# Kernel tuning notes

Hardware: AMD Instinct MI355X
Metric: run time of the kernel (lower is better)

The kernel has to match this reference:

```python
import math
import jax
import jax.numpy as jnp
import numpy as np
from jax import lax

B, L, D_MODEL, N_HEADS, C = 4, 2048, 512, 8, 1
D_HEAD = D_MODEL // N_HEADS


def setup_inputs() -> dict:
    key = jax.random.key(0)
    ks = jax.random.split(key, 7)
    s = 0.02  # stand-in for glorot init scale
    return {
        "queries": jax.random.normal(ks[0], (B, L, D_MODEL), jnp.float32),
        "keys": jax.random.normal(ks[1], (B, L, D_MODEL), jnp.float32),
        "values": jax.random.normal(ks[2], (B, L, D_MODEL), jnp.float32),
        "wq": jax.random.normal(ks[3], (D_MODEL, D_MODEL), jnp.float32) * s,
        "wk": jax.random.normal(ks[4], (D_MODEL, D_MODEL), jnp.float32) * s,
        "wv": jax.random.normal(ks[5], (D_MODEL, D_MODEL), jnp.float32) * s,
        "wo": jax.random.normal(ks[6], (D_MODEL, D_MODEL), jnp.float32) * s,
    }


def reference(queries, keys, values, wq, wk, wv, wo):
    b, len_q, _ = queries.shape
    len_k = keys.shape[1]
    # QKV projections, split into heads: [B, H, L, Dh]
    Q = (queries @ wq).reshape(b, len_q, N_HEADS, D_HEAD).transpose(0, 2, 1, 3)
    K = (keys @ wk).reshape(b, len_k, N_HEADS, D_HEAD).transpose(0, 2, 1, 3)
    V = (values @ wv).reshape(b, len_k, N_HEADS, D_HEAD).transpose(0, 2, 1, 3)
    # full O(L^2) correlation as in the original, then mean over heads & query idx
    corr = jnp.einsum("bhid,bhjd->bhij", Q, K)  # [B, H, Lq, Lk]
    mean_corr = corr.mean(axis=(1, 2))  # [B, Lk]
    # top-k delay selection (k = max(1, int(c * log(Lq))), static at trace time)
    k = max(1, int(C * math.log(max(2, len_q))))
    topk_vals, topk_idx = lax.top_k(mean_corr, k)  # [B, k]
    weights = jax.nn.softmax(topk_vals, axis=-1)  # [B, k]
    # vectorized circular roll: rolled[b,i,h,t,d] = V[b,h,(t+delay_bi) % L, d]
    idx = (jnp.arange(len_k)[None, None, :] + topk_idx[:, :, None]) % len_k  # [B,k,L]
    gathered = jnp.take_along_axis(
        V[:, None],  # [B, 1, H, L, Dh]
        idx[:, :, None, :, None],  # [B, k, 1, L, 1]
        axis=3,
    )  # [B, k, H, L, Dh]
    agg = jnp.einsum("bk,bkhld->bhld", weights.astype(V.dtype), gathered)
    out = agg.transpose(0, 2, 1, 3).reshape(b, len_q, D_MODEL) @ wo
    return out
```

## Files before the change

### kernel.cpp

```cpp
#include <hip/hip_runtime.h>
#include <hip/hip_bf16.h>

#define DMODEL 512
#define LEN 2048
#define NBATCH 4
#define TOPK 7
#define LDK 40

typedef __attribute__((ext_vector_type(8))) short short8;
typedef __attribute__((ext_vector_type(4))) float floatx4;

__device__ __forceinline__ float b2f(ushort h) {
  union { uint u; float f; } c; c.u = ((uint)h) << 16; return c.f;
}
__device__ __forceinline__ ushort f2b(float f) {
  union { float f; uint u; } c; c.f = f;
  uint u = c.u;
  uint r = (u + 0x7fffu + ((u >> 16) & 1u)) >> 16;
  return (ushort)r;
}

__device__ __forceinline__ float ld1(const void* p, size_t i, int bf) {
  return bf ? b2f(((const ushort*)p)[i]) : ((const float*)p)[i];
}
__device__ __forceinline__ void ld4v(const void* p, size_t i, int bf, float* o) {
  if (bf) {
    uint2 v = *(const uint2*)((const ushort*)p + i);
    const ushort* s = (const ushort*)&v;
#pragma unroll
    for (int j = 0; j < 4; ++j) o[j] = b2f(s[j]);
  } else {
    float4 a = *(const float4*)((const float*)p + i);
    o[0] = a.x; o[1] = a.y; o[2] = a.z; o[3] = a.w;
  }
}
__device__ __forceinline__ void ld8v(const void* p, size_t i, int bf, float* o) {
  if (bf) {
    uint4 v = *(const uint4*)((const ushort*)p + i);
    const ushort* s = (const ushort*)&v;
#pragma unroll
    for (int j = 0; j < 8; ++j) o[j] = b2f(s[j]);
  } else {
    float4 a = *(const float4*)((const float*)p + i);
    float4 b = *(const float4*)((const float*)p + i + 4);
    o[0] = a.x; o[1] = a.y; o[2] = a.z; o[3] = a.w;
    o[4] = b.x; o[5] = b.y; o[6] = b.z; o[7] = b.w;
  }
}

__device__ __forceinline__ int detect_bf16(const void* probe) {
  __shared__ int s_flag;
  int t = threadIdx.x;
  if (t < 64) {
    const uint4* p = (const uint4*)probe;
    uint4 a = p[t * 2];
    uint4 b = p[t * 2 + 1];
    uint w[8] = {a.x, a.y, a.z, a.w, b.x, b.y, b.z, b.w};
    int c = 0;
#pragma unroll
    for (int j = 0; j < 8; ++j) {
      uint e = (w[j] >> 7) & 0xFFu;
      c += (e < 90u || e > 140u) ? 1 : 0;
    }
#pragma unroll
    for (int off = 32; off > 0; off >>= 1) c += __shfl_down(c, off);
    if (t == 0) s_flag = (c < 50) ? 1 : 0;
  }
  __syncthreads();
  return s_flag;
}

__global__ __launch_bounds__(256) void prep_k(
    const void* __restrict__ queries, const void* __restrict__ values,
    const void* __restrict__ wv, const void* __restrict__ wo,
    const void* __restrict__ probe,
    float* __restrict__ P, ushort* __restrict__ VB, ushort* __restrict__ W2T) {
  __shared__ ushort As[64 * LDK];
  __shared__ ushort Bs[64 * LDK];
  __shared__ ushort Ts[64 * 72];
  int bf = detect_bf16(probe);
  int blk = blockIdx.x;
  int t = threadIdx.x;
  if (blk < 256) {
    int b = blk >> 6, c = blk & 63;
    size_t base = (((size_t)b * LEN + (size_t)c * 32) << 9) + t;
    float a0 = 0.f, a1 = 0.f;
#pragma unroll 8
    for (int l = 0; l < 32; ++l) {
      a0 += ld1(queries, base + ((size_t)l << 9), bf);
      a1 += ld1(queries, base + ((size_t)l << 9) + 256, bf);
    }
    P[(size_t)blk * DMODEL + t] = a0;
    P[(size_t)blk * DMODEL + t + 256] = a1;
  } else if (blk < 2304) {
    int r = (blk - 256) * 4 + (t >> 6);
    int lane = t & 63;
    float v[8];
    ld8v(values, ((size_t)r << 9) + lane * 8, bf, v);
    union { ushort o[8]; uint4 u; } pk;
#pragma unroll
    for (int j = 0; j < 8; ++j) pk.o[j] = f2b(v[j]);
    *(uint4*)(VB + ((size_t)r << 9) + lane * 8) = pk.u;
  } else {
    int wb = blk - 2304;
    int n0 = (wb & 7) * 64, m0 = (wb >> 3) * 64;
    int w = t >> 6, lane = t & 63;
    int quad = lane >> 4, l16 = lane & 15;
    floatx4 acc[4] = {{0,0,0,0},{0,0,0,0},{0,0,0,0},{0,0,0,0}};
    int am = t >> 2, ak = (t & 3) * 8;
    int kp = t >> 4, nb = (t & 15) * 4;
    for (int k0 = 0; k0 < DMODEL; k0 += 32) {
      float a8[8];
      ld8v(wv, (size_t)(m0 + am) * DMODEL + k0 + ak, bf, a8);
      union { ushort s[8]; uint4 v; } ap;
#pragma unroll
      for (int j = 0; j < 8; ++j) ap.s[j] = f2b(a8[j]);
      *(uint4*)(&As[am * LDK + ak]) = ap.v;
      float b0[4], b1[4];
      ld4v(wo, (size_t)(k0 + 2 * kp) * DMODEL + n0 + nb, bf, b0);
      ld4v(wo, (size_t)(k0 + 2 * kp + 1) * DMODEL + n0 + nb, bf, b1);
#pragma unroll
      for (int i = 0; i < 4; ++i) {
        ushort2 pr; pr.x = f2b(b0[i]); pr.y = f2b(b1[i]);
        *(ushort2*)(&Bs[(nb + i) * LDK + 2 * kp]) = pr;
      }
      __syncthreads();
      short8 af = *(const short8*)(&As[(w * 16 + l16) * LDK + quad * 8]);
#pragma unroll
      for (int c = 0; c < 4; ++c) {
        short8 bfr = *(const short8*)(&Bs[(c * 16 + l16) * LDK + quad * 8]);
        acc[c] = __builtin_amdgcn_mfma_f32_16x16x32_bf16(af, bfr, acc[c], 0, 0, 0);
      }
      __syncthreads();
    }
#pragma unroll
    for (int c = 0; c < 4; ++c) {
      int cl = c * 16 + l16;
#pragma unroll
      for (int r = 0; r < 4; ++r)
        Ts[cl * 72 + (w * 16 + quad * 4 + r)] = f2b(acc[c][r]);
    }
    __syncthreads();
    int nl = t >> 2, ch = t & 3;
    uint4 v0 = *(const uint4*)(&Ts[nl * 72 + ch * 16]);
    uint4 v1 = *(const uint4*)(&Ts[nl * 72 + ch * 16 + 8]);
    ushort* dst = W2T + (size_t)(n0 + nl) * DMODEL + m0 + ch * 16;
    *(uint4*)dst = v0;
    *(uint4*)(dst + 8) = v1;
  }
}

__global__ __launch_bounds__(256) void qbar_k(
    const float* __restrict__ P, const void* __restrict__ wq,
    float* __restrict__ qb) {
  __shared__ float qs[DMODEL];
  __shared__ float red[4][64];
  int bf = detect_bf16(wq);
  int b = blockIdx.x >> 3, g = blockIdx.x & 7;
  int t = threadIdx.x;
  for (int d = t; d < DMODEL; d += 256) {
    float a = 0.f;
#pragma unroll
    for (int c = 0; c < 64; ++c) a += P[(size_t)(b * 64 + c) * DMODEL + d];
    qs[d] = a;
  }
  __syncthreads();
  int part = t >> 6, jl = t & 63;
  int j = g * 64 + jl;
  float acc = 0.f;
  int d0 = part * 128;
#pragma unroll 8
  for (int d = d0; d < d0 + 128; ++d)
    acc += qs[d] * ld1(wq, (size_t)d * DMODEL + j, bf);
  red[part][jl] = acc;
  __syncthreads();
  if (part == 0)
    qb[(size_t)b * DMODEL + j] = red[0][jl] + red[1][jl] + red[2][jl] + red[3][jl];
}

__global__ __launch_bounds__(256) void u_k(
    const float* __restrict__ qb, const void* __restrict__ wk,
    float* __restrict__ u, const void* __restrict__ probe) {
  int bf = detect_bf16(probe);
  int gw = (blockIdx.x * 256 + threadIdx.x) >> 6;
  int lane = threadIdx.x & 63;
  int b = gw >> 9, t = gw & 511;
  float kv[8];
  ld8v(wk, (size_t)t * DMODEL + lane * 8, bf, kv);
  const float* qbb = qb + (size_t)b * DMODEL + lane * 8;
  float acc = 0.f;
#pragma unroll
  for (int i = 0; i < 8; ++i) acc += kv[i] * qbb[i];
#pragma unroll
  for (int off = 32; off > 0; off >>= 1) acc += __shfl_down(acc, off);
  if (lane == 0) u[(size_t)b * DMODEL + t] = acc;
}

__global__ __launch_bounds__(256) void mean_corr_k(
    const void* __restrict__ keys, const float* __restrict__ u,
    float* __restrict__ mc, const void* __restrict__ probe) {
  int bf = detect_bf16(probe);
  int wid = (blockIdx.x * 256 + threadIdx.x) >> 6;
  int lane = threadIdx.x & 63;
  int b = wid >> 11, j = wid & (LEN - 1);
  float kv[8];
  ld8v(keys, (((size_t)b * LEN + j) << 9) + lane * 8, bf, kv);
  const float* ub = u + (size_t)b * DMODEL + lane * 8;
  float acc = 0.f;
#pragma unroll
  for (int i = 0; i < 8; ++i) acc += kv[i] * ub[i];
#pragma unroll
  for (int off = 32; off > 0; off >>= 1) acc += __shfl_down(acc, off);
  if (lane == 0) mc[(size_t)b * LEN + j] = acc * (1.f / 16384.f);
}

__global__ void topk_softmax(const float* __restrict__ mc,
                             float* __restrict__ wts, int* __restrict__ dls) {
  __shared__ float vals[LEN];
  __shared__ float rv[4];
  __shared__ int ri[4];
  __shared__ float bv_s[TOPK];
  __shared__ int bi_s[TOPK];
  int b = blockIdx.x, t = threadIdx.x;
  for (int i = t; i < LEN; i += 256) vals[i] = mc[(size_t)b * LEN + i];
  __syncthreads();
  for (int it = 0; it < TOPK; ++it) {
    float bv = -3.0e38f; int bi = 0;
#pragma unroll
    for (int c = 0; c < LEN / 256; ++c) {
      int i = t + c * 256;
      float v = vals[i];
      if (v > bv) { bv = v; bi = i; }
    }
#pragma unroll
    for (int off = 32; off > 0; off >>= 1) {
      float ov = __shfl_down(bv, off);
      int   oi = __shfl_down(bi, off);
      if (ov > bv || (ov == bv && oi < bi)) { bv = ov; bi = oi; }
    }
    if ((t & 63) == 0) { rv[t >> 6] = bv; ri[t >> 6] = bi; }
    __syncthreads();
    if (t == 0) {
      float fv = rv[0]; int fi = ri[0];
      for (int w = 1; w < 4; ++w)
        if (rv[w] > fv || (rv[w] == fv && ri[w] < fi)) { fv = rv[w]; fi = ri[w]; }
      bv_s[it] = fv; bi_s[it] = fi;
      vals[fi] = -3.0e38f;
    }
    __syncthreads();
  }
  if (t == 0) {
    float m = bv_s[0];
    float e[TOPK], s = 0.f;
#pragma unroll
    for (int i = 0; i < TOPK; ++i) { e[i] = __expf(bv_s[i] - m); s += e[i]; }
    float inv = 1.f / s;
#pragma unroll
    for (int i = 0; i < TOPK; ++i) {
      wts[b * 8 + i] = e[i] * inv;
      dls[b * 8 + i] = bi_s[i];
    }
  }
}

__global__ __launch_bounds__(256) void mix_k(
    const ushort* __restrict__ VB, const float* __restrict__ wts,
    const int* __restrict__ dls, ushort* __restrict__ Amix) {
  int t = threadIdx.x;
  int row = blockIdx.x * 4 + (t >> 6);
  int lane = t & 63;
  int b = row >> 11, l = row & (LEN - 1);
  float w[TOPK]; int dl[TOPK];
#pragma unroll
  for (int i = 0; i < TOPK; ++i) { w[i] = wts[b * 8 + i]; dl[i] = dls[b * 8 + i]; }
  float acc[8] = {0,0,0,0,0,0,0,0};
#pragma unroll
  for (int i = 0; i < TOPK; ++i) {
    int src = (l + dl[i]) & (LEN - 1);
    uint4 v = *(const uint4*)(VB + (((size_t)b * LEN + src) << 9) + lane * 8);
    const ushort* vs = (const ushort*)&v;
#pragma unroll
    for (int j = 0; j < 8; ++j) acc[j] += w[i] * b2f(vs[j]);
  }
  union { ushort o[8]; uint4 v; } pk;
#pragma unroll
  for (int j = 0; j < 8; ++j) pk.o[j] = f2b(acc[j]);
  *(uint4*)(Amix + ((size_t)row << 9) + lane * 8) = pk.v;
}

__global__ __launch_bounds__(256) void gemm_out(
    const ushort* __restrict__ Amix, const ushort* __restrict__ W2T,
    void* __restrict__ out, const void* __restrict__ probe) {
  __shared__ ushort As[128 * LDK];
  __shared__ ushort Bs[128 * LDK];
  int bf = detect_bf16(probe);
  int t = threadIdx.x;
  int n0 = blockIdx.x * 128, m0 = blockIdx.y * 128;
  int w = t >> 6, lane = t & 63;
  int quad = lane >> 4, l16 = lane & 15;
  int wr = (w & 1) * 64, wc = (w >> 1) * 64;
  floatx4 acc[4][4];
#pragma unroll
  for (int r = 0; r < 4; ++r)
#pragma unroll
    for (int c = 0; c < 4; ++c) acc[r][c] = (floatx4){0, 0, 0, 0};
  int sr = t >> 2, sc = (t & 3) * 8;

  for (int k0 = 0; k0 < DMODEL; k0 += 32) {
    *(uint4*)(&As[sr * LDK + sc])        = *(const uint4*)(Amix + (size_t)(m0 + sr) * DMODEL + k0 + sc);
    *(uint4*)(&As[(sr + 64) * LDK + sc]) = *(const uint4*)(Amix + (size_t)(m0 + sr + 64) * DMODEL + k0 + sc);
    *(uint4*)(&Bs[sr * LDK + sc])        = *(const uint4*)(W2T + (size_t)(n0 + sr) * DMODEL + k0 + sc);
    *(uint4*)(&Bs[(sr + 64) * LDK + sc]) = *(const uint4*)(W2T + (size_t)(n0 + sr + 64) * DMODEL + k0 + sc);
    __syncthreads();
    short8 af[4], bfg[4];
#pragma unroll
    for (int r = 0; r < 4; ++r)
      af[r] = *(const short8*)(&As[(wr + r * 16 + l16) * LDK + quad * 8]);
#pragma unroll
    for (int c = 0; c < 4; ++c)
      bfg[c] = *(const short8*)(&Bs[(wc + c * 16 + l16) * LDK + quad * 8]);
#pragma unroll
    for (int r = 0; r < 4; ++r)
#pragma unroll
      for (int c = 0; c < 4; ++c)
        acc[r][c] = __builtin_amdgcn_mfma_f32_16x16x32_bf16(af[r], bfg[c], acc[r][c], 0, 0, 0);
    __syncthreads();
  }
#pragma unroll
  for (int r = 0; r < 4; ++r) {
    int row = m0 + wr + r * 16 + quad * 4;
#pragma unroll
    for (int c = 0; c < 4; ++c) {
      int col = n0 + wc + c * 16 + l16;
#pragma unroll
      for (int rr = 0; rr < 4; ++rr) {
        size_t oidx = (size_t)(row + rr) * DMODEL + col;
        float v = acc[r][c][rr];
        if (bf) ((ushort*)out)[oidx] = f2b(v);
        else    ((float*)out)[oidx] = v;
      }
    }
  }
}

extern "C" void kernel_launch(void* const* d_in, const int* in_sizes, int n_in,
                              void* d_out, int out_size, void* d_ws, size_t ws_size,
                              hipStream_t stream) {
  const void* queries = d_in[0];
  const void* keys    = d_in[1];
  const void* values  = d_in[2];
  const void* wq      = d_in[3];
  const void* wk      = d_in[4];
  const void* wv      = d_in[5];
  const void* wo      = d_in[6];

  char* ws = (char*)d_ws;
  float*  P    = (float*)(ws + 0);
  ushort* W2T  = (ushort*)(ws + 524288);
  float*  QB   = (float*)(ws + 1048576);
  float*  U    = (float*)(ws + 1056768);
  float*  MC   = (float*)(ws + 1064960);
  float*  WT   = (float*)(ws + 1097728);
  int*    DL   = (int*)  (ws + 1097856);
  ushort* VB   = (ushort*)(ws + 2097152);
  ushort* AMIX = (ushort*)(ws + 10485760);

  prep_k<<<2368, 256, 0, stream>>>(queries, values, wv, wo, wq, P, VB, W2T);
  qbar_k<<<NBATCH * 8, 256, 0, stream>>>(P, wq, QB);
  u_k<<<NBATCH * 512 / 4, 256, 0, stream>>>(QB, wk, U, wq);
  mean_corr_k<<<NBATCH * LEN / 4, 256, 0, stream>>>(keys, U, MC, wq);
  topk_softmax<<<NBATCH, 256, 0, stream>>>(MC, WT, DL);
  mix_k<<<NBATCH * LEN / 4, 256, 0, stream>>>(VB, WT, DL, AMIX);
  gemm_out<<<dim3(4, 64), 256, 0, stream>>>(AMIX, W2T, d_out, wq);
}
```

Baseline: 167.1 us.

## Precompute Wk·Wqᵀ, merge qbar/u kernels, fuse top-k into mix

```diff
diff --git a/kernel.cpp b/kernel.cpp
--- a/kernel.cpp
+++ b/kernel.cpp
@@ -72,40 +72,21 @@
 
 __global__ __launch_bounds__(256) void prep_k(
     const void* __restrict__ queries, const void* __restrict__ values,
+    const void* __restrict__ wq, const void* __restrict__ wk,
     const void* __restrict__ wv, const void* __restrict__ wo,
-    const void* __restrict__ probe,
-    float* __restrict__ P, ushort* __restrict__ VB, ushort* __restrict__ W2T) {
+    float* __restrict__ P, ushort* __restrict__ VB,
+    ushort* __restrict__ W2T, float* __restrict__ M) {
   __shared__ ushort As[64 * LDK];
   __shared__ ushort Bs[64 * LDK];
   __shared__ ushort Ts[64 * 72];
-  int bf = detect_bf16(probe);
+  int bf = detect_bf16(wq);
   int blk = blockIdx.x;
   int t = threadIdx.x;
-  if (blk < 256) {
-    int b = blk >> 6, c = blk & 63;
-    size_t base = (((size_t)b * LEN + (size_t)c * 32) << 9) + t;
-    float a0 = 0.f, a1 = 0.f;
-#pragma unroll 8
-    for (int l = 0; l < 32; ++l) {
-      a0 += ld1(queries, base + ((size_t)l << 9), bf);
-      a1 += ld1(queries, base + ((size_t)l << 9) + 256, bf);
-    }
-    P[(size_t)blk * DMODEL + t] = a0;
-    P[(size_t)blk * DMODEL + t + 256] = a1;
-  } else if (blk < 2304) {
-    int r = (blk - 256) * 4 + (t >> 6);
-    int lane = t & 63;
-    float v[8];
-    ld8v(values, ((size_t)r << 9) + lane * 8, bf, v);
-    union { ushort o[8]; uint4 u; } pk;
-#pragma unroll
-    for (int j = 0; j < 8; ++j) pk.o[j] = f2b(v[j]);
-    *(uint4*)(VB + ((size_t)r << 9) + lane * 8) = pk.u;
-  } else {
-    int wb = blk - 2304;
-    int n0 = (wb & 7) * 64, m0 = (wb >> 3) * 64;
-    int w = t >> 6, lane = t & 63;
-    int quad = lane >> 4, l16 = lane & 15;
+  int w = t >> 6, lane = t & 63;
+  int quad = lane >> 4, l16 = lane & 15;
+
+  if (blk < 64) {
+    int n0 = (blk & 7) * 64, m0 = (blk >> 3) * 64;
     floatx4 acc[4] = {{0,0,0,0},{0,0,0,0},{0,0,0,0},{0,0,0,0}};
     int am = t >> 2, ak = (t & 3) * 8;
     int kp = t >> 4, nb = (t & 15) * 4;
@@ -147,17 +128,67 @@
     ushort* dst = W2T + (size_t)(n0 + nl) * DMODEL + m0 + ch * 16;
     *(uint4*)dst = v0;
     *(uint4*)(dst + 8) = v1;
-  }
-}
-
-__global__ __launch_bounds__(256) void qbar_k(
-    const float* __restrict__ P, const void* __restrict__ wq,
-    float* __restrict__ qb) {
+  } else if (blk < 128) {
+    int wb = blk - 64;
+    int m0 = (wb >> 3) * 64, n0 = (wb & 7) * 64;
+    floatx4 acc[4] = {{0,0,0,0},{0,0,0,0},{0,0,0,0},{0,0,0,0}};
+    int am = t >> 2, ak = (t & 3) * 8;
+    for (int k0 = 0; k0 < DMODEL; k0 += 32) {
+      float a8[8], b8[8];
+      ld8v(wk, (size_t)(m0 + am) * DMODEL + k0 + ak, bf, a8);
+      ld8v(wq, (size_t)(n0 + am) * DMODEL + k0 + ak, bf, b8);
+      union { ushort s[8]; uint4 v; } ap, bp;
+#pragma unroll
+      for (int j = 0; j < 8; ++j) { ap.s[j] = f2b(a8[j]); bp.s[j] = f2b(b8[j]); }
+      *(uint4*)(&As[am * LDK + ak]) = ap.v;
+      *(uint4*)(&Bs[am * LDK + ak]) = bp.v;
+      __syncthreads();
+      short8 af = *(const short8*)(&As[(w * 16 + l16) * LDK + quad * 8]);
+#pragma unroll
+      for (int c = 0; c < 4; ++c) {
+        short8 bfr = *(const short8*)(&Bs[(c * 16 + l16) * LDK + quad * 8]);
+        acc[c] = __builtin_amdgcn_mfma_f32_16x16x32_bf16(af, bfr, acc[c], 0, 0, 0);
+      }
+      __syncthreads();
+    }
+    int mrow = m0 + w * 16 + quad * 4;
+#pragma unroll
+    for (int c = 0; c < 4; ++c) {
+      int col = n0 + c * 16 + l16;
+#pragma unroll
+      for (int r = 0; r < 4; ++r)
+        M[(size_t)(mrow + r) * DMODEL + col] = acc[c][r];
+    }
+  } else if (blk < 384) {
+    int idx = blk - 128;
+    int b = idx >> 6, c = idx & 63;
+    size_t base = (((size_t)b * LEN + (size_t)c * 32) << 9) + t;
+    float a0 = 0.f, a1 = 0.f;
+#pragma unroll 8
+    for (int l = 0; l < 32; ++l) {
+      a0 += ld1(queries, base + ((size_t)l << 9), bf);
+      a1 += ld1(queries, base + ((size_t)l << 9) + 256, bf);
+    }
+    P[(size_t)idx * DMODEL + t] = a0;
+    P[(size_t)idx * DMODEL + t + 256] = a1;
+  } else {
+    int r = (blk - 384) * 4 + w;
+    float v[8];
+    ld8v(values, ((size_t)r << 9) + lane * 8, bf, v);
+    union { ushort o[8]; uint4 u; } pk;
+#pragma unroll
+    for (int j = 0; j < 8; ++j) pk.o[j] = f2b(v[j]);
+    *(uint4*)(VB + ((size_t)r << 9) + lane * 8) = pk.u;
+  }
+}
+
+__global__ __launch_bounds__(256) void u_all(
+    const float* __restrict__ P, const float* __restrict__ M,
+    float* __restrict__ U) {
   __shared__ float qs[DMODEL];
-  __shared__ float red[4][64];
-  int bf = detect_bf16(wq);
-  int b = blockIdx.x >> 3, g = blockIdx.x & 7;
-  int t = threadIdx.x;
+  int blk = blockIdx.x, t = threadIdx.x;
+  int b = blk >> 5, g = blk & 31;
+  int w = t >> 6, lane = t & 63;
   for (int d = t; d < DMODEL; d += 256) {
     float a = 0.f;
 #pragma unroll
@@ -165,35 +196,19 @@
     qs[d] = a;
   }
   __syncthreads();
-  int part = t >> 6, jl = t & 63;
-  int j = g * 64 + jl;
-  float acc = 0.f;
-  int d0 = part * 128;
-#pragma unroll 8
-  for (int d = d0; d < d0 + 128; ++d)
-    acc += qs[d] * ld1(wq, (size_t)d * DMODEL + j, bf);
-  red[part][jl] = acc;
-  __syncthreads();
-  if (part == 0)
-    qb[(size_t)b * DMODEL + j] = red[0][jl] + red[1][jl] + red[2][jl] + red[3][jl];
-}
-
-__global__ __launch_bounds__(256) void u_k(
-    const float* __restrict__ qb, const void* __restrict__ wk,
-    float* __restrict__ u, const void* __restrict__ probe) {
-  int bf = detect_bf16(probe);
-  int gw = (blockIdx.x * 256 + threadIdx.x) >> 6;
-  int lane = threadIdx.x & 63;
-  int b = gw >> 9, t = gw & 511;
-  float kv[8];
-  ld8v(wk, (size_t)t * DMODEL + lane * 8, bf, kv);
-  const float* qbb = qb + (size_t)b * DMODEL + lane * 8;
-  float acc = 0.f;
-#pragma unroll
-  for (int i = 0; i < 8; ++i) acc += kv[i] * qbb[i];
-#pragma unroll
-  for (int off = 32; off > 0; off >>= 1) acc += __shfl_down(acc, off);
-  if (lane == 0) u[(size_t)b * DMODEL + t] = acc;
+  const float* q8 = qs + lane * 8;
+#pragma unroll
+  for (int i = 0; i < 4; ++i) {
+    int tt = g * 16 + w * 4 + i;
+    const float* mr = M + (size_t)tt * DMODEL + lane * 8;
+    float4 m0 = *(const float4*)mr;
+    float4 m1 = *(const float4*)(mr + 4);
+    float acc = m0.x * q8[0] + m0.y * q8[1] + m0.z * q8[2] + m0.w * q8[3]
+              + m1.x * q8[4] + m1.y * q8[5] + m1.z * q8[6] + m1.w * q8[7];
+#pragma unroll
+    for (int off = 32; off > 0; off >>= 1) acc += __shfl_down(acc, off);
+    if (lane == 0) U[(size_t)b * DMODEL + tt] = acc;
+  }
 }
 
 __global__ __launch_bounds__(256) void mean_corr_k(
@@ -214,15 +229,20 @@
   if (lane == 0) mc[(size_t)b * LEN + j] = acc * (1.f / 16384.f);
 }
 
-__global__ void topk_softmax(const float* __restrict__ mc,
-                             float* __restrict__ wts, int* __restrict__ dls) {
+__global__ __launch_bounds__(256) void topk_mix(
+    const float* __restrict__ MC, const ushort* __restrict__ VB,
+    ushort* __restrict__ Amix) {
   __shared__ float vals[LEN];
   __shared__ float rv[4];
   __shared__ int ri[4];
-  __shared__ float bv_s[TOPK];
-  __shared__ int bi_s[TOPK];
-  int b = blockIdx.x, t = threadIdx.x;
-  for (int i = t; i < LEN; i += 256) vals[i] = mc[(size_t)b * LEN + i];
+  __shared__ float bw[TOPK];
+  __shared__ int biA[TOPK];
+  __shared__ float wsm[8];
+  __shared__ int dsm[8];
+  int blk = blockIdx.x, t = threadIdx.x;
+  int w = t >> 6, lane = t & 63;
+  int b = blk >> 7;
+  for (int i = t; i < LEN; i += 256) vals[i] = MC[(size_t)b * LEN + i];
   __syncthreads();
   for (int it = 0; it < TOPK; ++it) {
     float bv = -3.0e38f; int bi = 0;
@@ -238,54 +258,47 @@
       int   oi = __shfl_down(bi, off);
       if (ov > bv || (ov == bv && oi < bi)) { bv = ov; bi = oi; }
     }
-    if ((t & 63) == 0) { rv[t >> 6] = bv; ri[t >> 6] = bi; }
+    if (lane == 0) { rv[w] = bv; ri[w] = bi; }
     __syncthreads();
     if (t == 0) {
       float fv = rv[0]; int fi = ri[0];
-      for (int w = 1; w < 4; ++w)
-        if (rv[w] > fv || (rv[w] == fv && ri[w] < fi)) { fv = rv[w]; fi = ri[w]; }
-      bv_s[it] = fv; bi_s[it] = fi;
+      for (int x = 1; x < 4; ++x)
+        if (rv[x] > fv || (rv[x] == fv && ri[x] < fi)) { fv = rv[x]; fi = ri[x]; }
+      bw[it] = fv; biA[it] = fi;
       vals[fi] = -3.0e38f;
     }
     __syncthreads();
   }
   if (t == 0) {
-    float m = bv_s[0];
+    float m = bw[0];
     float e[TOPK], s = 0.f;
 #pragma unroll
-    for (int i = 0; i < TOPK; ++i) { e[i] = __expf(bv_s[i] - m); s += e[i]; }
+    for (int i = 0; i < TOPK; ++i) { e[i] = __expf(bw[i] - m); s += e[i]; }
     float inv = 1.f / s;
 #pragma unroll
+    for (int i = 0; i < TOPK; ++i) { wsm[i] = e[i] * inv; dsm[i] = biA[i]; }
+  }
+  __syncthreads();
+  float w7[TOPK]; int dl7[TOPK];
+#pragma unroll
+  for (int i = 0; i < TOPK; ++i) { w7[i] = wsm[i]; dl7[i] = dsm[i]; }
+#pragma unroll
+  for (int half = 0; half < 4; ++half) {
+    int l = (blk & 127) * 16 + half * 4 + w;
+    float acc[8] = {0,0,0,0,0,0,0,0};
+#pragma unroll
     for (int i = 0; i < TOPK; ++i) {
-      wts[b * 8 + i] = e[i] * inv;
-      dls[b * 8 + i] = bi_s[i];
-    }
-  }
-}
-
-__global__ __launch_bounds__(256) void mix_k(
-    const ushort* __restrict__ VB, const float* __restrict__ wts,
-    const int* __restrict__ dls, ushort* __restrict__ Amix) {
-  int t = threadIdx.x;
-  int row = blockIdx.x * 4 + (t >> 6);
-  int lane = t & 63;
-  int b = row >> 11, l = row & (LEN - 1);
-  float w[TOPK]; int dl[TOPK];
-#pragma unroll
-  for (int i = 0; i < TOPK; ++i) { w[i] = wts[b * 8 + i]; dl[i] = dls[b * 8 + i]; }
-  float acc[8] = {0,0,0,0,0,0,0,0};
-#pragma unroll
-  for (int i = 0; i < TOPK; ++i) {
-    int src = (l + dl[i]) & (LEN - 1);
-    uint4 v = *(const uint4*)(VB + (((size_t)b * LEN + src) << 9) + lane * 8);
-    const ushort* vs = (const ushort*)&v;
-#pragma unroll
-    for (int j = 0; j < 8; ++j) acc[j] += w[i] * b2f(vs[j]);
-  }
-  union { ushort o[8]; uint4 v; } pk;
-#pragma unroll
-  for (int j = 0; j < 8; ++j) pk.o[j] = f2b(acc[j]);
-  *(uint4*)(Amix + ((size_t)row << 9) + lane * 8) = pk.v;
+      int src = (l + dl7[i]) & (LEN - 1);
+      uint4 v = *(const uint4*)(VB + (((size_t)b * LEN + src) << 9) + lane * 8);
+      const ushort* vs = (const ushort*)&v;
+#pragma unroll
+      for (int j = 0; j < 8; ++j) acc[j] += w7[i] * b2f(vs[j]);
+    }
+    union { ushort o[8]; uint4 v; } pk;
+#pragma unroll
+    for (int j = 0; j < 8; ++j) pk.o[j] = f2b(acc[j]);
+    *(uint4*)(Amix + (((size_t)b * LEN + l) << 9) + lane * 8) = pk.v;
+  }
 }
 
 __global__ __launch_bounds__(256) void gemm_out(
@@ -305,7 +318,6 @@
 #pragma unroll
     for (int c = 0; c < 4; ++c) acc[r][c] = (floatx4){0, 0, 0, 0};
   int sr = t >> 2, sc = (t & 3) * 8;
-
   for (int k0 = 0; k0 < DMODEL; k0 += 32) {
     *(uint4*)(&As[sr * LDK + sc])        = *(const uint4*)(Amix + (size_t)(m0 + sr) * DMODEL + k0 + sc);
     *(uint4*)(&As[(sr + 64) * LDK + sc]) = *(const uint4*)(Amix + (size_t)(m0 + sr + 64) * DMODEL + k0 + sc);
@@ -357,19 +369,15 @@
   char* ws = (char*)d_ws;
   float*  P    = (float*)(ws + 0);
   ushort* W2T  = (ushort*)(ws + 524288);
-  float*  QB   = (float*)(ws + 1048576);
-  float*  U    = (float*)(ws + 1056768);
-  float*  MC   = (float*)(ws + 1064960);
-  float*  WT   = (float*)(ws + 1097728);
-  int*    DL   = (int*)  (ws + 1097856);
-  ushort* VB   = (ushort*)(ws + 2097152);
-  ushort* AMIX = (ushort*)(ws + 10485760);
-
-  prep_k<<<2368, 256, 0, stream>>>(queries, values, wv, wo, wq, P, VB, W2T);
-  qbar_k<<<NBATCH * 8, 256, 0, stream>>>(P, wq, QB);
-  u_k<<<NBATCH * 512 / 4, 256, 0, stream>>>(QB, wk, U, wq);
+  float*  M    = (float*)(ws + 1048576);
+  float*  U    = (float*)(ws + 2097152);
+  float*  MC   = (float*)(ws + 2105344);
+  ushort* VB   = (ushort*)(ws + 4194304);
+  ushort* AMIX = (ushort*)(ws + 12582912);
+
+  prep_k<<<2432, 256, 0, stream>>>(queries, values, wq, wk, wv, wo, P, VB, W2T, M);
+  u_all<<<128, 256, 0, stream>>>(P, M, U);
   mean_corr_k<<<NBATCH * LEN / 4, 256, 0, stream>>>(keys, U, MC, wq);
-  topk_softmax<<<NBATCH, 256, 0, stream>>>(MC, WT, DL);
-  mix_k<<<NBATCH * LEN / 4, 256, 0, stream>>>(VB, WT, DL, AMIX);
+  topk_mix<<<512, 256, 0, stream>>>(MC, VB, AMIX);
   gemm_out<<<dim3(4, 64), 256, 0, stream>>>(AMIX, W2T, d_out, wq);
 }
```

Result: faster. 155.2 us (-7.1%).
